# Performance work log

Measured on AMD Instinct MI355X. Metric: run time of the kernel, lower is better.

The kernel has to match this reference:

```python
import jax, jax.numpy as jnp
import numpy as np
import math

D_MODEL = 256
N_HEADS = 4
D_K = D_MODEL // N_HEADS
N_LAYERS = 4
PAD_ID = 0
LN_EPS = 1e-5


def _posenc(seq_len, d_model):
    pos = jnp.arange(seq_len, dtype=jnp.float32)[:, None]
    div = jnp.exp(jnp.arange(0, d_model, 2, dtype=jnp.float32) * (-math.log(10000.0) / d_model))
    pe = jnp.zeros((seq_len, d_model), dtype=jnp.float32)
    pe = pe.at[:, 0::2].set(jnp.sin(pos * div))
    pe = pe.at[:, 1::2].set(jnp.cos(pos * div))
    return pe  # (S, D)


def _layernorm(x, g, b):
    mu = jnp.mean(x, axis=-1, keepdims=True)
    var = jnp.mean((x - mu) ** 2, axis=-1, keepdims=True)
    return (x - mu) / jnp.sqrt(var + LN_EPS) * g + b


def _attention(x, mask_b11s, Wq, bq, Wk, bk, Wv, bv, Wo, bo):
    B, S, D = x.shape
    q = (x @ Wq + bq).reshape(B, S, N_HEADS, D_K)
    k = (x @ Wk + bk).reshape(B, S, N_HEADS, D_K)
    v = (x @ Wv + bv).reshape(B, S, N_HEADS, D_K)
    scores = jnp.einsum('bqhd,bkhd->bhqk', q, k) / math.sqrt(D_K)
    scores = jnp.where(mask_b11s, scores, -jnp.inf)
    attn = jax.nn.softmax(scores, axis=-1)
    out = jnp.einsum('bhqk,bkhd->bqhd', attn, v).reshape(B, S, D)
    return out @ Wo + bo


def setup_inputs() -> dict:
    key = jax.random.key(0)
    ks = jax.random.split(key, 16)
    B, S, V, D, F, L, C = 16, 2048, 32, D_MODEL, 1024, N_LAYERS, 10
    input_ids = jax.random.randint(ks[0], (B, S), 0, V, dtype=jnp.int64)
    emb = jax.random.normal(ks[1], (V, D), jnp.float32) * (D ** -0.5)
    emb = emb.at[PAD_ID].set(0.0)  # padding_idx
    sc = 0.05
    inp = {
        'input_ids': input_ids,
        'emb': emb,
        'Wq': jax.random.normal(ks[2], (L, D, D), jnp.float32) * sc,
        'bq': jnp.zeros((L, D), jnp.float32),
        'Wk': jax.random.normal(ks[3], (L, D, D), jnp.float32) * sc,
        'bk': jnp.zeros((L, D), jnp.float32),
        'Wv': jax.random.normal(ks[4], (L, D, D), jnp.float32) * sc,
        'bv': jnp.zeros((L, D), jnp.float32),
        'Wo': jax.random.normal(ks[5], (L, D, D), jnp.float32) * sc,
        'bo': jnp.zeros((L, D), jnp.float32),
        'g1': jnp.ones((L, D), jnp.float32),
        'be1': jnp.zeros((L, D), jnp.float32),
        'W1': jax.random.normal(ks[6], (L, D, F), jnp.float32) * sc,
        'b1': jnp.zeros((L, F), jnp.float32),
        'W2': jax.random.normal(ks[7], (L, F, D), jnp.float32) * sc,
        'b2': jnp.zeros((L, D), jnp.float32),
        'g2': jnp.ones((L, D), jnp.float32),
        'be2': jnp.zeros((L, D), jnp.float32),
        'Wc': jax.random.normal(ks[8], (D, C), jnp.float32) * sc,
        'bc': jnp.zeros((C,), jnp.float32),
    }
    return inp


def reference(input_ids, emb, Wq, bq, Wk, bk, Wv, bv, Wo, bo,
              g1, be1, W1, b1, W2, b2, g2, be2, Wc, bc):
    B, S = input_ids.shape
    attn_mask = (input_ids != PAD_ID)                      # (B, S) bool
    mask_b11s = attn_mask[:, None, None, :]                # (B,1,1,S)
    x = emb[input_ids] * math.sqrt(D_MODEL)                # (B,S,D)
    x = x + _posenc(S, D_MODEL)[None]
    for l in range(N_LAYERS):
        a = _attention(x, mask_b11s, Wq[l], bq[l], Wk[l], bk[l], Wv[l], bv[l], Wo[l], bo[l])
        x = _layernorm(x + a, g1[l], be1[l])
        ff = jax.nn.relu(x @ W1[l] + b1[l]) @ W2[l] + b2[l]
        x = _layernorm(x + ff, g2[l], be2[l])
    # mean pooling over non-pad tokens
    m = attn_mask.astype(jnp.float32)[:, :, None]          # (B,S,1)
    pooled = jnp.sum(x * m, axis=1) / jnp.clip(jnp.sum(m, axis=1), 1e-9)
    logits = pooled @ Wc + bc                              # (B, num_classes)
    return logits
```

## Files before the change

### kernel.cpp

```cpp
#include <hip/hip_runtime.h>
#include <hip/hip_bf16.h>
#include <math.h>

#define D_MODEL 256
#define NHEADS 4
#define DK 64
#define NLAYERS 4
#define FFDIM 1024
#define BB 16
#define SS 2048
#define NTOK (BB*SS)

#define QSCALE 0.18033688011112042f
#define MASKNEG -30000.0f

typedef __attribute__((ext_vector_type(8))) short bf16x8;
typedef __attribute__((ext_vector_type(4))) short s16x4;
typedef __attribute__((ext_vector_type(4))) float f32x4;

__device__ __forceinline__ short f2bf(float f) {
    __hip_bfloat16 h = __float2bfloat16(f);
    return *reinterpret_cast<short*>(&h);
}

__global__ void embed_kernel(const int* __restrict__ ids, const float* __restrict__ emb,
                             float* __restrict__ x, short* __restrict__ xb) {
    int idx = blockIdx.x * 256 + threadIdx.x;
    int tok = idx >> 8;
    int d   = idx & 255;
    int s   = tok & (SS - 1);
    int id  = ids[tok];
    float e = emb[id * D_MODEL + d] * 16.0f;
    float i2 = (float)((d >> 1) << 1);
    float div = expf(i2 * (-9.210340371976184f / 256.0f));
    float ang = (float)s * div;
    float pe = (d & 1) ? cosf(ang) : sinf(ang);
    float val = e + pe;
    x[idx] = val;
    xb[idx] = f2bf(val);
}

__global__ void wprep_kernel(const float* __restrict__ Wq, const float* __restrict__ Wk,
                             const float* __restrict__ Wv, const float* __restrict__ Wo,
                             const float* __restrict__ W1, const float* __restrict__ W2,
                             short* __restrict__ wqkv, short* __restrict__ wto,
                             short* __restrict__ w1t, short* __restrict__ w2t) {
    int wid = blockIdx.y, l = blockIdx.z, tile = blockIdx.x;
    int K = (wid == 5) ? 1024 : 256;
    int M = (wid == 4) ? 1024 : 256;
    int tiles = (K >> 6) * (M >> 6);
    if (tile >= tiles) return;
    const float* src; short* dst;
    float scale = (wid == 0) ? QSCALE : 1.0f;
    switch (wid) {
        case 0: src = Wq; dst = wqkv + (size_t)l*196608;            break;
        case 1: src = Wk; dst = wqkv + (size_t)l*196608 + 65536;    break;
        case 2: src = Wv; dst = wqkv + (size_t)l*196608 + 131072;   break;
        case 3: src = Wo; dst = wto + (size_t)l*65536;              break;
        case 4: src = W1; dst = w1t + (size_t)l*262144;             break;
        default: src = W2; dst = w2t + (size_t)l*262144;            break;
    }
    src += (size_t)l * K * M;
    int tm = tile % (M >> 6), tk = tile / (M >> 6);

    __shared__ short t_s[64][68];
    int tid = threadIdx.x;
    #pragma unroll
    for (int u = 0; u < 16; ++u) {
        int e = tid + u * 256;
        int r = e >> 6, c = e & 63;
        t_s[c][r] = f2bf(src[(size_t)(tk*64 + r) * M + tm*64 + c] * scale);
    }
    __syncthreads();
    #pragma unroll
    for (int u = 0; u < 4; ++u) {
        int e = tid + u * 256;
        int r = e >> 4, c4 = (e & 15) * 4;
        s16x4 v;
        v[0] = t_s[r][c4]; v[1] = t_s[r][c4+1]; v[2] = t_s[r][c4+2]; v[3] = t_s[r][c4+3];
        *(s16x4*)&dst[(size_t)(tm*64 + r) * K + tk*64 + c4] = v;
    }
}

__global__ void bprep_kernel(const float* __restrict__ bq, const float* __restrict__ bk,
                             const float* __restrict__ bv, float* __restrict__ bqkv) {
    int idx = blockIdx.x * 256 + threadIdx.x;
    if (idx >= NLAYERS * 768) return;
    int l = idx / 768, j = idx % 768;
    float v;
    if (j < 256) v = bq[l*256 + j] * QSCALE;
    else if (j < 512) v = bk[l*256 + j - 256];
    else v = bv[l*256 + j - 512];
    bqkv[idx] = v;
}

template<int RELU>
__global__ __launch_bounds__(256) void gemm_bf16_kernel(
        const short* __restrict__ A, const short* __restrict__ Wt,
        const float* __restrict__ bias, short* __restrict__ Cout,
        int N, int K, int M) {
    __shared__ short A_s[128][72];
    __shared__ short B_s[128][72];
    int tid = threadIdx.x;
    int w = tid >> 6, lane = tid & 63;
    int lr = lane & 15, lg = lane >> 4;
    int wr = w >> 1, wc = w & 1;
    int rowBase = blockIdx.x * 128;
    int colBase = blockIdx.y * 128;

    f32x4 acc[4][4];
    #pragma unroll
    for (int m = 0; m < 4; ++m)
        #pragma unroll
        for (int n = 0; n < 4; ++n)
            acc[m][n] = (f32x4){0.f, 0.f, 0.f, 0.f};

    for (int kt = 0; kt < K; kt += 64) {
        #pragma unroll
        for (int u = 0; u < 4; ++u) {
            int e = tid + u * 256;
            int r = e >> 3, c8 = (e & 7) * 8;
            *(bf16x8*)&A_s[r][c8] = *(const bf16x8*)(A + (size_t)(rowBase + r) * K + kt + c8);
        }
        #pragma unroll
        for (int u = 0; u < 4; ++u) {
            int e = tid + u * 256;
            int r = e >> 3, c8 = (e & 7) * 8;
            *(bf16x8*)&B_s[r][c8] = *(const bf16x8*)(Wt + (size_t)(colBase + r) * K + kt + c8);
        }
        __syncthreads();
        #pragma unroll
        for (int ks = 0; ks < 2; ++ks) {
            bf16x8 af[4], bfr[4];
            #pragma unroll
            for (int m = 0; m < 4; ++m)
                af[m] = *(const bf16x8*)&A_s[wr*64 + m*16 + lr][ks*32 + lg*8];
            #pragma unroll
            for (int n = 0; n < 4; ++n)
                bfr[n] = *(const bf16x8*)&B_s[wc*64 + n*16 + lr][ks*32 + lg*8];
            #pragma unroll
            for (int m = 0; m < 4; ++m)
                #pragma unroll
                for (int n = 0; n < 4; ++n)
                    acc[m][n] = __builtin_amdgcn_mfma_f32_16x16x32_bf16(af[m], bfr[n], acc[m][n], 0, 0, 0);
        }
        __syncthreads();
    }

    #pragma unroll
    for (int m = 0; m < 4; ++m) {
        int row = rowBase + wr*64 + m*16 + lg*4;
        #pragma unroll
        for (int n = 0; n < 4; ++n) {
            int col = colBase + wc*64 + n*16 + lr;
            float bv = bias[col];
            #pragma unroll
            for (int r = 0; r < 4; ++r) {
                float vv = acc[m][n][r] + bv;
                if (RELU) vv = fmaxf(vv, 0.0f);
                Cout[(size_t)(row + r) * M + col] = f2bf(vv);
            }
        }
    }
}

__global__ __launch_bounds__(256) void gemm_ln_kernel(
        const short* __restrict__ A, const short* __restrict__ Wt,
        const float* __restrict__ bias, const float* __restrict__ resid,
        const float* __restrict__ g, const float* __restrict__ be,
        float* __restrict__ xf, short* __restrict__ xb, int K) {
    __shared__ short A_s[64][72];
    __shared__ short B_s[256][72];
    __shared__ float red_s[2][4][64];
    __shared__ float mu_s[64], rs_s[64];
    int tid = threadIdx.x;
    int w = tid >> 6, lane = tid & 63;
    int lr = lane & 15, lg = lane >> 4;
    int rowBase = blockIdx.x * 64;
    int colW = w * 64;

    f32x4 acc[4][4];
    #pragma unroll
    for (int m = 0; m < 4; ++m)
        #pragma unroll
        for (int n = 0; n < 4; ++n)
            acc[m][n] = (f32x4){0.f, 0.f, 0.f, 0.f};

    for (int kt = 0; kt < K; kt += 64) {
        #pragma unroll
        for (int u = 0; u < 2; ++u) {
            int e = tid + u * 256;
            int r = e >> 3, c8 = (e & 7) * 8;
            *(bf16x8*)&A_s[r][c8] = *(const bf16x8*)(A + (size_t)(rowBase + r) * K + kt + c8);
        }
        #pragma unroll
        for (int u = 0; u < 8; ++u) {
            int e = tid + u * 256;
            int r = e >> 3, c8 = (e & 7) * 8;
            *(bf16x8*)&B_s[r][c8] = *(const bf16x8*)(Wt + (size_t)r * K + kt + c8);
        }
        __syncthreads();
        #pragma unroll
        for (int ks = 0; ks < 2; ++ks) {
            bf16x8 af[4], bfr[4];
            #pragma unroll
            for (int m = 0; m < 4; ++m)
                af[m] = *(const bf16x8*)&A_s[m*16 + lr][ks*32 + lg*8];
            #pragma unroll
            for (int n = 0; n < 4; ++n)
                bfr[n] = *(const bf16x8*)&B_s[colW + n*16 + lr][ks*32 + lg*8];
            #pragma unroll
            for (int m = 0; m < 4; ++m)
                #pragma unroll
                for (int n = 0; n < 4; ++n)
                    acc[m][n] = __builtin_amdgcn_mfma_f32_16x16x32_bf16(af[m], bfr[n], acc[m][n], 0, 0, 0);
        }
        __syncthreads();
    }

    #pragma unroll
    for (int m = 0; m < 4; ++m) {
        #pragma unroll
        for (int n = 0; n < 4; ++n) {
            int col = colW + n*16 + lr;
            float bv = bias[col];
            #pragma unroll
            for (int r = 0; r < 4; ++r) {
                int row = rowBase + m*16 + lg*4 + r;
                acc[m][n][r] += bv + resid[(size_t)row * 256 + col];
            }
        }
    }
    #pragma unroll
    for (int m = 0; m < 4; ++m) {
        #pragma unroll
        for (int r = 0; r < 4; ++r) {
            float sum = acc[m][0][r] + acc[m][1][r] + acc[m][2][r] + acc[m][3][r];
            float sq  = acc[m][0][r]*acc[m][0][r] + acc[m][1][r]*acc[m][1][r]
                      + acc[m][2][r]*acc[m][2][r] + acc[m][3][r]*acc[m][3][r];
            #pragma unroll
            for (int off = 1; off < 16; off <<= 1) {
                sum += __shfl_xor(sum, off);
                sq  += __shfl_xor(sq, off);
            }
            if (lr == 0) {
                red_s[0][w][m*16 + lg*4 + r] = sum;
                red_s[1][w][m*16 + lg*4 + r] = sq;
            }
        }
    }
    __syncthreads();
    if (tid < 64) {
        float s = red_s[0][0][tid] + red_s[0][1][tid] + red_s[0][2][tid] + red_s[0][3][tid];
        float q = red_s[1][0][tid] + red_s[1][1][tid] + red_s[1][2][tid] + red_s[1][3][tid];
        float mu = s * (1.0f/256.0f);
        float var = q * (1.0f/256.0f) - mu*mu;
        mu_s[tid] = mu;
        rs_s[tid] = rsqrtf(var + 1e-5f);
    }
    __syncthreads();
    #pragma unroll
    for (int m = 0; m < 4; ++m) {
        #pragma unroll
        for (int n = 0; n < 4; ++n) {
            int col = colW + n*16 + lr;
            float gv = g[col], bev = be[col];
            #pragma unroll
            for (int r = 0; r < 4; ++r) {
                int rloc = m*16 + lg*4 + r;
                int row = rowBase + rloc;
                float o = (acc[m][n][r] - mu_s[rloc]) * rs_s[rloc] * gv + bev;
                xf[(size_t)row * 256 + col] = o;
                xb[(size_t)row * 256 + col] = f2bf(o);
            }
        }
    }
}

__global__ __launch_bounds__(256) void flash_mfma_kernel(
        const short* __restrict__ qkv, const int* __restrict__ ids,
        short* __restrict__ out) {
    __shared__ short k_s[64][72];
    __shared__ short vt_s[64][72];
    __shared__ short p_s[4][16][72];
    __shared__ float madd_s[64];

    int bid = blockIdx.x;
    int work = (bid & 7) * 128 + (bid >> 3);
    int qb = work & 15, h = (work >> 4) & 3, b = work >> 6;

    int tid = threadIdx.x;
    int w = tid >> 6, lane = tid & 63;
    int lr = lane & 15, lg = lane >> 4;
    int g = lr >> 2;

    const short* qp = qkv + (size_t)b * SS * 768 + h * DK;
    const short* kp = qp + 256;
    const short* vp = qp + 512;

    bf16x8 qf[2][2];
    #pragma unroll
    for (int s = 0; s < 2; ++s) {
        int qrow = qb*128 + w*32 + s*16 + lr;
        #pragma unroll
        for (int ks = 0; ks < 2; ++ks)
            qf[s][ks] = *(const bf16x8*)(qp + (size_t)qrow * 768 + lg*8 + ks*32);
    }

    f32x4 o[2][4];
    float m_i[2] = {-1e30f, -1e30f}, l_i[2] = {0.0f, 0.0f};
    #pragma unroll
    for (int s = 0; s < 2; ++s)
        #pragma unroll
        for (int dt = 0; dt < 4; ++dt)
            o[s][dt] = (f32x4){0.f, 0.f, 0.f, 0.f};

    bf16x8 kr[2], vr[2];
    int idv = 1;
    #pragma unroll
    for (int u = 0; u < 2; ++u) {
        int e = tid + u * 256;
        int r = e >> 3, c8 = (e & 7) * 8;
        kr[u] = *(const bf16x8*)(kp + (size_t)r * 768 + c8);
        vr[u] = *(const bf16x8*)(vp + (size_t)r * 768 + c8);
    }
    if (tid < 64) idv = ids[b*SS + tid];

    for (int kb = 0; kb < SS/64; ++kb) {
        __syncthreads();
        #pragma unroll
        for (int u = 0; u < 2; ++u) {
            int e = tid + u * 256;
            int r = e >> 3, c8 = (e & 7) * 8;
            *(bf16x8*)&k_s[r][c8] = kr[u];
            #pragma unroll
            for (int j = 0; j < 8; ++j) {
                int col = c8 + j;
                vt_s[col][((((r >> 3) ^ (col >> 3)) << 3) | (r & 7))] = vr[u][j];
            }
        }
        if (tid < 64)
            madd_s[tid] = (idv != 0) ? 0.0f : MASKNEG;
        if (kb + 1 < SS/64) {
            #pragma unroll
            for (int u = 0; u < 2; ++u) {
                int e = tid + u * 256;
                int r = e >> 3, c8 = (e & 7) * 8;
                kr[u] = *(const bf16x8*)(kp + (size_t)((kb+1)*64 + r) * 768 + c8);
                vr[u] = *(const bf16x8*)(vp + (size_t)((kb+1)*64 + r) * 768 + c8);
            }
            if (tid < 64) idv = ids[b*SS + (kb+1)*64 + tid];
        }
        __syncthreads();

        f32x4 madd4[4];
        #pragma unroll
        for (int t = 0; t < 4; ++t)
            madd4[t] = *(const f32x4*)&madd_s[16*t + 4*lg];

        f32x4 sc[2][4];
        __builtin_amdgcn_s_setprio(1);
        #pragma unroll
        for (int t = 0; t < 4; ++t) {
            bf16x8 kf0 = *(const bf16x8*)&k_s[t*16 + lr][lg*8];
            bf16x8 kf1 = *(const bf16x8*)&k_s[t*16 + lr][lg*8 + 32];
            #pragma unroll
            for (int s = 0; s < 2; ++s) {
                f32x4 a = __builtin_amdgcn_mfma_f32_16x16x32_bf16(kf0, qf[s][0], madd4[t], 0, 0, 0);
                a = __builtin_amdgcn_mfma_f32_16x16x32_bf16(kf1, qf[s][1], a, 0, 0, 0);
                sc[s][t] = a;
            }
        }
        __builtin_amdgcn_s_setprio(0);

        #pragma unroll
        for (int s = 0; s < 2; ++s) {
            float mx = sc[s][0][0];
            #pragma unroll
            for (int t = 0; t < 4; ++t)
                #pragma unroll
                for (int r = 0; r < 4; ++r)
                    mx = fmaxf(mx, sc[s][t][r]);
            mx = fmaxf(mx, __shfl_xor(mx, 16));
            mx = fmaxf(mx, __shfl_xor(mx, 32));

            if (!__all(mx <= m_i[s])) {
                float mnew = fmaxf(m_i[s], mx);
                float alpha = __builtin_amdgcn_exp2f(m_i[s] - mnew);
                l_i[s] *= alpha;
                #pragma unroll
                for (int dt = 0; dt < 4; ++dt) o[s][dt] *= alpha;
                m_i[s] = mnew;
            }

            float rsum = 0.0f;
            float pv[4][4];
            #pragma unroll
            for (int t = 0; t < 4; ++t)
                #pragma unroll
                for (int r = 0; r < 4; ++r) {
                    float p = __builtin_amdgcn_exp2f(sc[s][t][r] - m_i[s]);
                    pv[t][r] = p;
                    rsum += p;
                }
            rsum += __shfl_xor(rsum, 16);
            rsum += __shfl_xor(rsum, 32);
            l_i[s] += rsum;

            #pragma unroll
            for (int t = 0; t < 4; ++t) {
                s16x4 pw;
                #pragma unroll
                for (int r = 0; r < 4; ++r) pw[r] = f2bf(pv[t][r]);
                *(s16x4*)&p_s[w][lr][16*(t ^ g) + 4*lg] = pw;
            }

            bf16x8 pa[2];
            #pragma unroll
            for (int ks = 0; ks < 2; ++ks) {
                int t0 = 2*ks + (lg >> 1);
                pa[ks] = *(const bf16x8*)&p_s[w][lr][16*(t0 ^ g) + 8*(lg & 1)];
            }
            __builtin_amdgcn_s_setprio(1);
            #pragma unroll
            for (int dt = 0; dt < 4; ++dt) {
                int col = dt*16 + lr;
                #pragma unroll
                for (int ks = 0; ks < 2; ++ks) {
                    bf16x8 va = *(const bf16x8*)&vt_s[col][(((ks*4 + lg) ^ (col >> 3)) << 3)];
                    o[s][dt] = __builtin_amdgcn_mfma_f32_16x16x32_bf16(va, pa[ks], o[s][dt], 0, 0, 0);
                }
            }
            __builtin_amdgcn_s_setprio(0);
        }
    }

    #pragma unroll
    for (int s = 0; s < 2; ++s) {
        float inv = 1.0f / l_i[s];
        int row = b*SS + qb*128 + w*32 + s*16 + lr;
        #pragma unroll
        for (int dt = 0; dt < 4; ++dt) {
            s16x4 ow;
            #pragma unroll
            for (int r = 0; r < 4; ++r) ow[r] = f2bf(o[s][dt][r] * inv);
            *(s16x4*)&out[(size_t)row * 256 + h*DK + dt*16 + 4*lg] = ow;
        }
    }
}

__global__ void pool1_kernel(const float* __restrict__ x, const int* __restrict__ ids,
                             float* __restrict__ partial) {
    int b = blockIdx.x >> 4, chunk = blockIdx.x & 15;
    int d = threadIdx.x;
    float acc = 0.0f;
    int s0 = chunk * 128;
    for (int s = s0; s < s0 + 128; ++s) {
        if (ids[b*SS + s] != 0) acc += x[(size_t)(b*SS + s) * D_MODEL + d];
    }
    partial[(size_t)(b*16 + chunk) * D_MODEL + d] = acc;
}

__global__ void pool2_kernel(const float* __restrict__ partial, const int* __restrict__ ids,
                             float* __restrict__ pooled) {
    int b = blockIdx.x;
    int d = threadIdx.x;
    float acc = 0.0f;
    for (int c = 0; c < 16; ++c) acc += partial[(size_t)(b*16 + c) * D_MODEL + d];
    int cnt = 0;
    for (int s = threadIdx.x; s < SS; s += 256) cnt += (ids[b*SS + s] != 0);
    __shared__ int cs[256];
    cs[threadIdx.x] = cnt;
    __syncthreads();
    for (int off = 128; off > 0; off >>= 1) {
        if (threadIdx.x < off) cs[threadIdx.x] += cs[threadIdx.x + off];
        __syncthreads();
    }
    float total = (float)cs[0];
    pooled[b * D_MODEL + d] = acc / fmaxf(total, 1e-9f);
}

__global__ void cls_kernel(const float* __restrict__ pooled, const float* __restrict__ Wc,
                           const float* __restrict__ bc, float* __restrict__ outp) {
    int t = threadIdx.x;
    if (t >= BB * 10) return;
    int b = t / 10, c = t % 10;
    float acc = bc[c];
    for (int d = 0; d < D_MODEL; ++d)
        acc += pooled[b * D_MODEL + d] * Wc[d * 10 + c];
    outp[t] = acc;
}

extern "C" void kernel_launch(void* const* d_in, const int* in_sizes, int n_in,
                              void* d_out, int out_size, void* d_ws, size_t ws_size,
                              hipStream_t stream) {
    const int*   ids = (const int*)  d_in[0];
    const float* emb = (const float*)d_in[1];
    const float* Wq  = (const float*)d_in[2];
    const float* bq  = (const float*)d_in[3];
    const float* Wk  = (const float*)d_in[4];
    const float* bk  = (const float*)d_in[5];
    const float* Wv  = (const float*)d_in[6];
    const float* bv  = (const float*)d_in[7];
    const float* Wo  = (const float*)d_in[8];
    const float* bo  = (const float*)d_in[9];
    const float* g1  = (const float*)d_in[10];
    const float* be1 = (const float*)d_in[11];
    const float* W1  = (const float*)d_in[12];
    const float* b1  = (const float*)d_in[13];
    const float* W2  = (const float*)d_in[14];
    const float* b2  = (const float*)d_in[15];
    const float* g2  = (const float*)d_in[16];
    const float* be2 = (const float*)d_in[17];
    const float* Wc  = (const float*)d_in[18];
    const float* bc  = (const float*)d_in[19];
    float* outp = (float*)d_out;

    const size_t TD = (size_t)NTOK * D_MODEL;
    float* ws   = (float*)d_ws;
    float* x    = ws;
    short* sb   = (short*)(ws + TD);
    short* xb   = sb;
    short* qkv  = sb + TD;
    short* t0   = sb + 4*TD;
    short* hh   = qkv;
    short* wqkv = sb + 5*TD;
    short* wto  = wqkv + (size_t)NLAYERS*196608;
    short* w1t  = wto  + (size_t)NLAYERS*65536;
    short* w2t  = w1t  + (size_t)NLAYERS*262144;
    float* bqkv = (float*)(w2t + (size_t)NLAYERS*262144);
    float* poolp = bqkv + NLAYERS*768;
    float* pooled = poolp + 65536;

    wprep_kernel<<<dim3(64, 6, NLAYERS), 256, 0, stream>>>(Wq, Wk, Wv, Wo, W1, W2,
                                                           wqkv, wto, w1t, w2t);
    bprep_kernel<<<12, 256, 0, stream>>>(bq, bk, bv, bqkv);
    embed_kernel<<<NTOK, 256, 0, stream>>>(ids, emb, x, xb);

    dim3 gQKV(NTOK/128, 768/128);
    dim3 gF1 (NTOK/128, FFDIM/128);

    for (int l = 0; l < NLAYERS; ++l) {
        gemm_bf16_kernel<0><<<gQKV, 256, 0, stream>>>(xb, wqkv + (size_t)l*196608, bqkv + l*768,
                                                      qkv, NTOK, D_MODEL, 768);
        flash_mfma_kernel<<<1024, 256, 0, stream>>>(qkv, ids, t0);
        gemm_ln_kernel<<<NTOK/64, 256, 0, stream>>>(t0, wto + (size_t)l*65536, bo + l*D_MODEL,
                                                    x, g1 + l*D_MODEL, be1 + l*D_MODEL,
                                                    x, xb, D_MODEL);
        gemm_bf16_kernel<1><<<gF1, 256, 0, stream>>>(xb, w1t + (size_t)l*262144, b1 + l*FFDIM,
                                                     hh, NTOK, D_MODEL, FFDIM);
        gemm_ln_kernel<<<NTOK/64, 256, 0, stream>>>(hh, w2t + (size_t)l*262144, b2 + l*D_MODEL,
                                                    x, g2 + l*D_MODEL, be2 + l*D_MODEL,
                                                    x, xb, FFDIM);
    }

    pool1_kernel<<<BB*16, 256, 0, stream>>>(x, ids, poolp);
    pool2_kernel<<<BB, 256, 0, stream>>>(poolp, ids, pooled);
    cls_kernel<<<1, 256, 0, stream>>>(pooled, Wc, bc, outp);
}
```

Before: 1.139 ms.

## Write V transposed from QKV GEMM and batch PV MFMAs across both query subtiles

The QKV GEMM epilogue now writes the V part directly into a per-(batch,head) transposed layout [D_K][S] in a new workspace buffer. The flash attention kernel can then load V^T tiles with plain vector stores to LDS instead of a scalar per-element transpose scatter. The PV stage is also restructured so P for both 16-row subtiles is staged first and each V fragment is reused for two MFMAs. The cost is an extra workspace buffer, strided 4-element stores in the GEMM epilogue, and doubled p_s shared memory.

New measurement: 1.085 ms. 4.8% less time.

```diff
diff --git a/kernel.cpp b/kernel.cpp
--- a/kernel.cpp
+++ b/kernel.cpp
@@ -94,11 +94,11 @@
     bqkv[idx] = v;
 }
 
-template<int RELU>
+template<int RELU, int VSPLIT>
 __global__ __launch_bounds__(256) void gemm_bf16_kernel(
         const short* __restrict__ A, const short* __restrict__ Wt,
         const float* __restrict__ bias, short* __restrict__ Cout,
-        int N, int K, int M) {
+        short* __restrict__ vt, int N, int K, int M) {
     __shared__ short A_s[128][72];
     __shared__ short B_s[128][72];
     int tid = threadIdx.x;
@@ -154,11 +154,20 @@
         for (int n = 0; n < 4; ++n) {
             int col = colBase + wc*64 + n*16 + lr;
             float bv = bias[col];
-            #pragma unroll
-            for (int r = 0; r < 4; ++r) {
-                float vv = acc[m][n][r] + bv;
-                if (RELU) vv = fmaxf(vv, 0.0f);
-                Cout[(size_t)(row + r) * M + col] = f2bf(vv);
+            if (VSPLIT && col >= 512) {
+                int hh = (col - 512) >> 6, dl = (col - 512) & 63;
+                int bb = row >> 11, s0 = row & 2047;
+                s16x4 ow;
+                #pragma unroll
+                for (int r = 0; r < 4; ++r) ow[r] = f2bf(acc[m][n][r] + bv);
+                *(s16x4*)&vt[((size_t)(bb * NHEADS + hh) * DK + dl) * SS + s0] = ow;
+            } else {
+                #pragma unroll
+                for (int r = 0; r < 4; ++r) {
+                    float vv = acc[m][n][r] + bv;
+                    if (RELU) vv = fmaxf(vv, 0.0f);
+                    Cout[(size_t)(row + r) * M + col] = f2bf(vv);
+                }
             }
         }
     }
@@ -278,11 +287,11 @@
 }
 
 __global__ __launch_bounds__(256) void flash_mfma_kernel(
-        const short* __restrict__ qkv, const int* __restrict__ ids,
-        short* __restrict__ out) {
+        const short* __restrict__ qkv, const short* __restrict__ vt_g,
+        const int* __restrict__ ids, short* __restrict__ out) {
     __shared__ short k_s[64][72];
     __shared__ short vt_s[64][72];
-    __shared__ short p_s[4][16][72];
+    __shared__ short p_s[4][32][72];
     __shared__ float madd_s[64];
 
     int bid = blockIdx.x;
@@ -296,7 +305,7 @@
 
     const short* qp = qkv + (size_t)b * SS * 768 + h * DK;
     const short* kp = qp + 256;
-    const short* vp = qp + 512;
+    const short* vtp = vt_g + (size_t)(b * NHEADS + h) * DK * SS;
 
     bf16x8 qf[2][2];
     #pragma unroll
@@ -315,14 +324,14 @@
         for (int dt = 0; dt < 4; ++dt)
             o[s][dt] = (f32x4){0.f, 0.f, 0.f, 0.f};
 
+    int r0 = tid >> 3, c8 = (tid & 7) * 8;
+
     bf16x8 kr[2], vr[2];
     int idv = 1;
     #pragma unroll
     for (int u = 0; u < 2; ++u) {
-        int e = tid + u * 256;
-        int r = e >> 3, c8 = (e & 7) * 8;
-        kr[u] = *(const bf16x8*)(kp + (size_t)r * 768 + c8);
-        vr[u] = *(const bf16x8*)(vp + (size_t)r * 768 + c8);
+        kr[u] = *(const bf16x8*)(kp + (size_t)(r0 + u*32) * 768 + c8);
+        vr[u] = *(const bf16x8*)(vtp + (size_t)(r0 + u*32) * SS + c8);
     }
     if (tid < 64) idv = ids[b*SS + tid];
 
@@ -330,24 +339,16 @@
         __syncthreads();
         #pragma unroll
         for (int u = 0; u < 2; ++u) {
-            int e = tid + u * 256;
-            int r = e >> 3, c8 = (e & 7) * 8;
-            *(bf16x8*)&k_s[r][c8] = kr[u];
-            #pragma unroll
-            for (int j = 0; j < 8; ++j) {
-                int col = c8 + j;
-                vt_s[col][((((r >> 3) ^ (col >> 3)) << 3) | (r & 7))] = vr[u][j];
-            }
+            *(bf16x8*)&k_s[r0 + u*32][c8] = kr[u];
+            *(bf16x8*)&vt_s[r0 + u*32][c8] = vr[u];
         }
         if (tid < 64)
             madd_s[tid] = (idv != 0) ? 0.0f : MASKNEG;
         if (kb + 1 < SS/64) {
             #pragma unroll
             for (int u = 0; u < 2; ++u) {
-                int e = tid + u * 256;
-                int r = e >> 3, c8 = (e & 7) * 8;
-                kr[u] = *(const bf16x8*)(kp + (size_t)((kb+1)*64 + r) * 768 + c8);
-                vr[u] = *(const bf16x8*)(vp + (size_t)((kb+1)*64 + r) * 768 + c8);
+                kr[u] = *(const bf16x8*)(kp + (size_t)((kb+1)*64 + r0 + u*32) * 768 + c8);
+                vr[u] = *(const bf16x8*)(vtp + (size_t)(r0 + u*32) * SS + (kb+1)*64 + c8);
             }
             if (tid < 64) idv = ids[b*SS + (kb+1)*64 + tid];
         }
@@ -412,27 +413,29 @@
                 s16x4 pw;
                 #pragma unroll
                 for (int r = 0; r < 4; ++r) pw[r] = f2bf(pv[t][r]);
-                *(s16x4*)&p_s[w][lr][16*(t ^ g) + 4*lg] = pw;
-            }
-
-            bf16x8 pa[2];
+                *(s16x4*)&p_s[w][s*16 + lr][16*(t ^ g) + 4*lg] = pw;
+            }
+        }
+
+        bf16x8 pa[2][2];
+        #pragma unroll
+        for (int s = 0; s < 2; ++s)
             #pragma unroll
             for (int ks = 0; ks < 2; ++ks) {
                 int t0 = 2*ks + (lg >> 1);
-                pa[ks] = *(const bf16x8*)&p_s[w][lr][16*(t0 ^ g) + 8*(lg & 1)];
-            }
-            __builtin_amdgcn_s_setprio(1);
-            #pragma unroll
-            for (int dt = 0; dt < 4; ++dt) {
-                int col = dt*16 + lr;
-                #pragma unroll
-                for (int ks = 0; ks < 2; ++ks) {
-                    bf16x8 va = *(const bf16x8*)&vt_s[col][(((ks*4 + lg) ^ (col >> 3)) << 3)];
-                    o[s][dt] = __builtin_amdgcn_mfma_f32_16x16x32_bf16(va, pa[ks], o[s][dt], 0, 0, 0);
-                }
-            }
-            __builtin_amdgcn_s_setprio(0);
-        }
+                pa[s][ks] = *(const bf16x8*)&p_s[w][s*16 + lr][16*(t0 ^ g) + 8*(lg & 1)];
+            }
+        __builtin_amdgcn_s_setprio(1);
+        #pragma unroll
+        for (int dt = 0; dt < 4; ++dt) {
+            #pragma unroll
+            for (int ks = 0; ks < 2; ++ks) {
+                bf16x8 va = *(const bf16x8*)&vt_s[dt*16 + lr][ks*32 + lg*8];
+                o[0][dt] = __builtin_amdgcn_mfma_f32_16x16x32_bf16(va, pa[0][ks], o[0][dt], 0, 0, 0);
+                o[1][dt] = __builtin_amdgcn_mfma_f32_16x16x32_bf16(va, pa[1][ks], o[1][dt], 0, 0, 0);
+            }
+        }
+        __builtin_amdgcn_s_setprio(0);
     }
 
     #pragma unroll
@@ -523,8 +526,9 @@
     short* xb   = sb;
     short* qkv  = sb + TD;
     short* t0   = sb + 4*TD;
+    short* vt_g = sb + 5*TD;
     short* hh   = qkv;
-    short* wqkv = sb + 5*TD;
+    short* wqkv = sb + 6*TD;
     short* wto  = wqkv + (size_t)NLAYERS*196608;
     short* w1t  = wto  + (size_t)NLAYERS*65536;
     short* w2t  = w1t  + (size_t)NLAYERS*262144;
@@ -541,14 +545,14 @@
     dim3 gF1 (NTOK/128, FFDIM/128);
 
     for (int l = 0; l < NLAYERS; ++l) {
-        gemm_bf16_kernel<0><<<gQKV, 256, 0, stream>>>(xb, wqkv + (size_t)l*196608, bqkv + l*768,
-                                                      qkv, NTOK, D_MODEL, 768);
-        flash_mfma_kernel<<<1024, 256, 0, stream>>>(qkv, ids, t0);
+        gemm_bf16_kernel<0,1><<<gQKV, 256, 0, stream>>>(xb, wqkv + (size_t)l*196608, bqkv + l*768,
+                                                        qkv, vt_g, NTOK, D_MODEL, 768);
+        flash_mfma_kernel<<<1024, 256, 0, stream>>>(qkv, vt_g, ids, t0);
         gemm_ln_kernel<<<NTOK/64, 256, 0, stream>>>(t0, wto + (size_t)l*65536, bo + l*D_MODEL,
                                                     x, g1 + l*D_MODEL, be1 + l*D_MODEL,
                                                     x, xb, D_MODEL);
-        gemm_bf16_kernel<1><<<gF1, 256, 0, stream>>>(xb, w1t + (size_t)l*262144, b1 + l*FFDIM,
-                                                     hh, NTOK, D_MODEL, FFDIM);
+        gemm_bf16_kernel<1,0><<<gF1, 256, 0, stream>>>(xb, w1t + (size_t)l*262144, b1 + l*FFDIM,
+                                                       hh, nullptr, NTOK, D_MODEL, FFDIM);
         gemm_ln_kernel<<<NTOK/64, 256, 0, stream>>>(hh, w2t + (size_t)l*262144, b2 + l*D_MODEL,
                                                     x, g2 + l*D_MODEL, be2 + l*D_MODEL,
                                                     x, xb, FFDIM);
```
